# Kernel tuning notes

Measured on AMD Instinct MI355X. Metric: run time of the kernel, lower is better.

## Reference

```python
import jax, jax.numpy as jnp
import numpy as np

N, R, C_IN, C_OUT, MODES = 8, 256, 64, 64, 16


def setup_inputs() -> dict:
    key = jax.random.key(0)
    k1, k2, k3, k4, k5 = jax.random.split(key, 5)
    # xavier-like scale used in the torch init: gain/(in*out)*sqrt(in+out) folded into std
    std = (1.0 / (C_IN * C_OUT)) * np.sqrt(2.0)  # small, keeps spectra sane
    return {
        "X": jax.random.normal(k1, (N, R, R, C_IN), dtype=jnp.float32),
        "W_res": jax.random.normal(k2, (C_IN, C_OUT), dtype=jnp.float32) / np.sqrt(C_IN),
        "b_res": jax.random.normal(k3, (C_OUT,), dtype=jnp.float32) * 0.01,
        "fw0": jax.random.normal(k4, (C_IN, C_OUT, MODES, MODES, 2), dtype=jnp.float32) * std,
        "fw1": jax.random.normal(k5, (C_IN, C_OUT, MODES, MODES, 2), dtype=jnp.float32) * std,
    }


def reference(X, W_res, b_res, fw0, fw1):
    # X: [N, r, r, in_dim]
    n, r, _, _ = X.shape
    modes = fw0.shape[2]
    out_dim = fw0.shape[1]

    res = X @ W_res + b_res  # [N, r, r, out_dim]  (dropout p=0.0 -> identity)

    Xc = jnp.transpose(X, (0, 3, 1, 2))  # [N, in, r, r]
    X_ft = jnp.fft.rfft2(Xc, s=(r, r), norm="ortho")  # [N, in, r, r//2+1] complex

    w0 = fw0[..., 0] + 1j * fw0[..., 1]  # [in, out, m, m] complex
    w1 = fw1[..., 0] + 1j * fw1[..., 1]

    top = jnp.einsum("bixy,ioxy->boxy", X_ft[:, :, :modes, :modes], w0)
    bot = jnp.einsum("bixy,ioxy->boxy", X_ft[:, :, r - modes :, :modes], w1)

    out_ft = jnp.zeros((n, out_dim, r, r // 2 + 1), dtype=X_ft.dtype)
    out_ft = out_ft.at[:, :, :modes, :modes].set(top)
    out_ft = out_ft.at[:, :, r - modes :, :modes].set(bot)

    Xo = jnp.fft.irfft2(out_ft, s=(r, r), norm="ortho")  # [N, out, r, r] real
    Xo = jnp.transpose(Xo, (0, 2, 3, 1))  # [N, r, r, out]
    return jax.nn.silu(Xo + res)
```

## Files before the change

kernel.cpp:

```cpp
#include <hip/hip_runtime.h>
#include <math.h>

#define RDIM 256
#define CIN 64
#define COUT 64
#define MODES 16
#define NB 8

typedef short short8 __attribute__((ext_vector_type(8)));
typedef float f32x4 __attribute__((ext_vector_type(4)));

__device__ __forceinline__ unsigned short f2b(float f) {
    unsigned u = __builtin_bit_cast(unsigned, f);
    unsigned r = (u + 0x7FFFu + ((u >> 16) & 1u)) >> 16;
    return (unsigned short)r;
}

__global__ __launch_bounds__(256) void k_tf(unsigned short* __restrict__ Tf2,
                                            unsigned short* __restrict__ T2) {
    int e = blockIdx.x * 256 + (int)threadIdx.x;
    if (e < 8192) {
        int kyc = e >> 8, k = e & 255;
        int S = k >> 3, j = k & 7;
        int w = S >> 3, h = (S >> 2) & 1, q = S & 3;
        int y = w * 64 + q + 4 * (h * 8 + j);
        int ky = kyc >> 1;
        int p = (ky * y) & 255;
        float ang = (float)p * (float)(2.0 * M_PI / 256.0);
        float sz, cz;
        sincosf(ang, &sz, &cz);
        Tf2[e] = f2b((kyc & 1) ? -sz : cz);
    } else {
        int f = e - 8192;
        int r = f >> 9, k = f & 511;
        int S = k >> 3, j = k & 7;
        int w = S >> 4, bp = (S >> 3) & 1, a = S & 7;
        int d = j >> 1, c = j & 1;
        int x = w * 64 + bp + 8 * a + 2 * d;
        int m = r >> 1, cc = r & 1;
        int kx = (m < 16) ? m : (m + 224);
        int p = (kx * x) & 255;
        float ang = (float)p * (float)(2.0 * M_PI / 256.0);
        float sz, cz;
        sincosf(ang, &sz, &cz);
        float val = (cc == 0) ? (c ? sz : cz) : (c ? cz : -sz);
        T2[f] = f2b(val * (1.0f / 256.0f));
    }
}

__global__ __launch_bounds__(256) void k_wt(const float* __restrict__ fw0,
                                            const float* __restrict__ fw1,
                                            float2* __restrict__ WT) {
    __shared__ float2 Ls[16][257];
    int blk = blockIdx.x;
    int arr = blk >> 8;
    int tile = blk & 255;
    const float2* s2 = (const float2*)(arr ? fw1 : fw0);
    int t = (int)threadIdx.x;
    for (int e = t; e < 4096; e += 256) {
        int oo = e >> 8;
        int q = e & 255;
        Ls[oo][q] = s2[(size_t)(tile * 16 + oo) * 256 + q];
    }
    __syncthreads();
    int i = (tile * 16) >> 6;
    int o0 = (tile * 16) & 63;
    for (int e = t; e < 4096; e += 256) {
        int oo = e & 15;
        int q = e >> 4;
        int mx = q >> 4, ky = q & 15;
        int m = arr * 16 + mx;
        WT[((size_t)(m * 16 + ky) * 64 + i) * 64 + o0 + oo] = Ls[oo][q];
    }
}

__global__ __launch_bounds__(256) void k_prep(const float* __restrict__ Wres,
                                              unsigned short* __restrict__ WbT,
                                              unsigned short* __restrict__ Tg,
                                              unsigned short* __restrict__ A2) {
    int e = blockIdx.x * 256 + (int)threadIdx.x;
    if (e < 4096) {
        int o = e >> 6, k = e & 63;
        WbT[o * 64 + k] = f2b(Wres[k * 64 + o]);
    } else if (e < 12288) {
        int f = e - 4096;
        int y = f >> 5, kk = f & 31, ky = kk >> 1;
        int p = (ky * y) & 255;
        float ang = (float)p * (float)(2.0 * M_PI / 256.0);
        float sz, cz;
        sincosf(ang, &sz, &cz);
        Tg[f] = f2b((kk & 1) ? -sz : cz);
    } else {
        int f = e - 12288;
        int comp = f >> 14, g = f & 16383;
        int x = g >> 6, k = g & 63;
        int m = k >> 1, c = k & 1;
        int kx = (m < 16) ? m : (m + 224);
        int p = (kx * x) & 255;
        float ang = (float)p * (float)(2.0 * M_PI / 256.0);
        float sz, cz;
        sincosf(ang, &sz, &cz);
        float val = (comp == 0) ? (c ? -sz : cz) : (c ? cz : sz);
        A2[f] = f2b(val);
    }
}

__global__ __launch_bounds__(256) void k_fwd_y(const float* __restrict__ X,
                                               const unsigned short* __restrict__ Tf,
                                               float2* __restrict__ A) {
    __shared__ short8 Xb[64 * 32];
    int b = blockIdx.x >> 8;
    int x = blockIdx.x & 255;
    int t = (int)threadIdx.x;
    int w = t >> 6;
    int l = t & 63;
    int q = l >> 4;
    int f4 = l & 15;
    int i0 = f4 * 4;

    const float4* X4 = (const float4*)(X + ((size_t)(b * 256 + x)) * 256 * 64);
#pragma unroll
    for (int h = 0; h < 2; h++) {
        float4 v[8];
#pragma unroll
        for (int n = 0; n < 8; n++) {
            int y = w * 64 + q + 4 * (h * 8 + n);
            v[n] = X4[y * 16 + f4];
        }
        const float* vf = (const float*)v;
        int s = w * 8 + h * 4 + q;
#pragma unroll
        for (int di = 0; di < 4; di++) {
            int i = i0 + di;
            short8 hb;
#pragma unroll
            for (int j = 0; j < 8; j++) hb[j] = (short)f2b(vf[j * 4 + di]);
            Xb[i * 32 + (s ^ (i & 7))] = hb;
        }
    }
    __syncthreads();

    int m16 = l & 15;
    int quad = l >> 4;
    int iRow = w * 16 + m16;
    int isw = iRow & 7;

    f32x4 acc0 = (f32x4){0.f, 0.f, 0.f, 0.f};
    f32x4 acc1 = (f32x4){0.f, 0.f, 0.f, 0.f};
    const unsigned short* T0 = Tf + (size_t)m16 * 256 + quad * 8;
#pragma unroll
    for (int ks = 0; ks < 8; ks++) {
        short8 a0 = *(const short8*)(T0 + ks * 32);
        short8 a1 = *(const short8*)(T0 + 4096 + ks * 32);
        short8 bfrag = Xb[iRow * 32 + ((ks * 4 + quad) ^ isw)];
        acc0 = __builtin_amdgcn_mfma_f32_16x16x32_bf16(a0, bfrag, acc0, 0, 0, 0);
        acc1 = __builtin_amdgcn_mfma_f32_16x16x32_bf16(a1, bfrag, acc1, 0, 0, 0);
    }

    float2* Ab = A + ((size_t)(b * 16) * 256 + x) * 64;
    int ky0 = quad * 2;
    Ab[(size_t)(ky0)     * 16384 + iRow] = make_float2(acc0[0], acc0[1]);
    Ab[(size_t)(ky0 + 1) * 16384 + iRow] = make_float2(acc0[2], acc0[3]);
    Ab[(size_t)(ky0 + 8) * 16384 + iRow] = make_float2(acc1[0], acc1[1]);
    Ab[(size_t)(ky0 + 9) * 16384 + iRow] = make_float2(acc1[2], acc1[3]);
}

__global__ __launch_bounds__(256) void k_fwd_x(const float2* __restrict__ A,
                                               const unsigned short* __restrict__ T2,
                                               float2* __restrict__ C) {
    __shared__ short8 Bs[64 * 64];
    int bi = blockIdx.x;
    int b = bi >> 4;
    int ky = bi & 15;
    int t = (int)threadIdx.x;
    int w = t >> 6, l = t & 63;
    int i2 = (l & 31) * 2;
    int bp = l >> 5;
    const float4* A4 = (const float4*)(A + ((size_t)(b * 16 + ky)) * 256 * 64);
#pragma unroll
    for (int a = 0; a < 8; a++) {
        float4 v[4];
#pragma unroll
        for (int d4 = 0; d4 < 4; d4++) {
            int xx = w * 64 + bp + 8 * a + 2 * d4;
            v[d4] = A4[xx * 32 + (l & 31)];
        }
        int S = w * 16 + bp * 8 + a;
        short8 h0, h1;
        h0[0] = (short)f2b(v[0].x); h0[1] = (short)f2b(v[0].y);
        h0[2] = (short)f2b(v[1].x); h0[3] = (short)f2b(v[1].y);
        h0[4] = (short)f2b(v[2].x); h0[5] = (short)f2b(v[2].y);
        h0[6] = (short)f2b(v[3].x); h0[7] = (short)f2b(v[3].y);
        h1[0] = (short)f2b(v[0].z); h1[1] = (short)f2b(v[0].w);
        h1[2] = (short)f2b(v[1].z); h1[3] = (short)f2b(v[1].w);
        h1[4] = (short)f2b(v[2].z); h1[5] = (short)f2b(v[2].w);
        h1[6] = (short)f2b(v[3].z); h1[7] = (short)f2b(v[3].w);
        Bs[i2 * 64 + (S ^ (i2 & 7))] = h0;
        Bs[(i2 + 1) * 64 + (S ^ ((i2 + 1) & 7))] = h1;
    }
    __syncthreads();

    int m16 = l & 15, quad = l >> 4;
    int iRow = w * 16 + m16;
    int isw = iRow & 7;
    f32x4 acc[4];
#pragma unroll
    for (int mt = 0; mt < 4; mt++) acc[mt] = (f32x4){0.f, 0.f, 0.f, 0.f};
    const unsigned short* Tp = T2 + (size_t)m16 * 512 + quad * 8;
#pragma unroll
    for (int ks = 0; ks < 16; ks++) {
        short8 bfrag = Bs[iRow * 64 + ((ks * 4 + quad) ^ isw)];
#pragma unroll
        for (int mt = 0; mt < 4; mt++) {
            short8 af = *(const short8*)(Tp + mt * 8192 + ks * 32);
            acc[mt] = __builtin_amdgcn_mfma_f32_16x16x32_bf16(af, bfrag, acc[mt], 0, 0, 0);
        }
    }

    float2* Cb = C + ((size_t)(b * 16 + ky)) * 32 * 64;
#pragma unroll
    for (int mt = 0; mt < 4; mt++) {
        int m0 = mt * 8 + quad * 2;
        Cb[(size_t)m0 * 64 + iRow]       = make_float2(acc[mt][0], acc[mt][1]);
        Cb[(size_t)(m0 + 1) * 64 + iRow] = make_float2(acc[mt][2], acc[mt][3]);
    }
}

__global__ __launch_bounds__(256) void k_mix(const float2* __restrict__ C,
                                             const float2* __restrict__ WT,
                                             float2* __restrict__ D) {
    __shared__ float2 Ws[64 * 64];
    __shared__ float2 Cs[8 * 64];
    __shared__ float2 red[4 * 8 * 64];
    int bi = blockIdx.x;
    int ky = bi >> 5;
    int m = bi & 31;
    int t = (int)threadIdx.x;
    const float4* Wsrc = (const float4*)(WT + ((size_t)(m * 16 + ky)) * 4096);
    float4* Wd = (float4*)Ws;
    for (int e = t; e < 2048; e += 256) Wd[e] = Wsrc[e];
    for (int e = t; e < 512; e += 256) {
        int b = e >> 6;
        int i = e & 63;
        Cs[e] = C[(((size_t)b * 16 + ky) * 32 + m) * 64 + i];
    }
    __syncthreads();
    int o = t & 63;
    int ig = t >> 6;
    float dr[8], di[8];
#pragma unroll
    for (int b = 0; b < 8; b++) { dr[b] = 0.f; di[b] = 0.f; }
    for (int i2 = ig * 16; i2 < ig * 16 + 16; i2++) {
        float2 w = Ws[i2 * 64 + o];
#pragma unroll
        for (int b = 0; b < 8; b++) {
            float2 c = Cs[b * 64 + i2];
            dr[b] += c.x * w.x - c.y * w.y;
            di[b] += c.x * w.y + c.y * w.x;
        }
    }
#pragma unroll
    for (int b = 0; b < 8; b++) red[(ig * 8 + b) * 64 + o] = make_float2(dr[b], di[b]);
    __syncthreads();
    for (int e = t; e < 512; e += 256) {
        int b = e >> 6;
        int oo = e & 63;
        float2 s = red[b * 64 + oo];
        float2 s1 = red[(8 + b) * 64 + oo];
        float2 s2 = red[(16 + b) * 64 + oo];
        float2 s3 = red[(24 + b) * 64 + oo];
        D[(((size_t)b * 16 + ky) * 32 + m) * 64 + oo] =
            make_float2((s.x + s1.x) + (s2.x + s3.x), (s.y + s1.y) + (s2.y + s3.y));
    }
}

__global__ __launch_bounds__(256) void k_inv_x(const float2* __restrict__ D,
                                               const unsigned short* __restrict__ A2,
                                               float2* __restrict__ G) {
    __shared__ short8 Bd[64 * 8];
    int bi = blockIdx.x;
    int b = bi >> 5;
    int ky = (bi >> 1) & 15;
    int xh = bi & 1;
    int t = (int)threadIdx.x;
    int w = t >> 6, l = t & 63;
    const float2* Dp = D + ((size_t)(b * 16 + ky)) * 32 * 64;
    float2 dv[8];
#pragma unroll
    for (int s = 0; s < 8; s++) dv[s] = Dp[(size_t)(w * 8 + s) * 64 + l];
    short8 h0, h1;
    h0[0] = (short)f2b(dv[0].x); h0[1] = (short)f2b(dv[0].y);
    h0[2] = (short)f2b(dv[1].x); h0[3] = (short)f2b(dv[1].y);
    h0[4] = (short)f2b(dv[2].x); h0[5] = (short)f2b(dv[2].y);
    h0[6] = (short)f2b(dv[3].x); h0[7] = (short)f2b(dv[3].y);
    h1[0] = (short)f2b(dv[4].x); h1[1] = (short)f2b(dv[4].y);
    h1[2] = (short)f2b(dv[5].x); h1[3] = (short)f2b(dv[5].y);
    h1[4] = (short)f2b(dv[6].x); h1[5] = (short)f2b(dv[6].y);
    h1[6] = (short)f2b(dv[7].x); h1[7] = (short)f2b(dv[7].y);
    int sl = l & 7;
    Bd[l * 8 + ((2 * w) ^ sl)]     = h0;
    Bd[l * 8 + ((2 * w + 1) ^ sl)] = h1;
    __syncthreads();

    int m16 = l & 15, quad = l >> 4;
    int x0 = xh * 128 + w * 32;
    f32x4 acc[2][4][2];
#pragma unroll
    for (int mt = 0; mt < 2; mt++)
#pragma unroll
        for (int nt = 0; nt < 4; nt++)
#pragma unroll
            for (int c = 0; c < 2; c++) acc[mt][nt][c] = (f32x4){0.f, 0.f, 0.f, 0.f};

#pragma unroll
    for (int ks = 0; ks < 2; ks++) {
        short8 ar[2], ai[2];
#pragma unroll
        for (int mt = 0; mt < 2; mt++) {
            int xr = x0 + mt * 16 + m16;
            ar[mt] = *(const short8*)(A2 + (size_t)xr * 64 + ks * 32 + quad * 8);
            ai[mt] = *(const short8*)(A2 + 16384 + (size_t)xr * 64 + ks * 32 + quad * 8);
        }
#pragma unroll
        for (int nt = 0; nt < 4; nt++) {
            int o = nt * 16 + m16;
            short8 bf = Bd[o * 8 + ((ks * 4 + quad) ^ (o & 7))];
#pragma unroll
            for (int mt = 0; mt < 2; mt++) {
                acc[mt][nt][0] = __builtin_amdgcn_mfma_f32_16x16x32_bf16(ar[mt], bf, acc[mt][nt][0], 0, 0, 0);
                acc[mt][nt][1] = __builtin_amdgcn_mfma_f32_16x16x32_bf16(ai[mt], bf, acc[mt][nt][1], 0, 0, 0);
            }
        }
    }

#pragma unroll
    for (int mt = 0; mt < 2; mt++)
#pragma unroll
        for (int nt = 0; nt < 4; nt++) {
            int o = nt * 16 + m16;
#pragma unroll
            for (int r = 0; r < 4; r++) {
                int x = x0 + mt * 16 + quad * 4 + r;
                G[((size_t)(b * 256 + x) * 16 + ky) * 64 + o] =
                    make_float2(acc[mt][nt][0][r], acc[mt][nt][1][r]);
            }
        }
}

__global__ __launch_bounds__(256) void k_out(const float* __restrict__ X,
                                             const float2* __restrict__ G,
                                             const unsigned short* __restrict__ WbT,
                                             const unsigned short* __restrict__ Tg,
                                             const float* __restrict__ bres,
                                             float* __restrict__ out) {
    __shared__ unsigned short Bsp[64 * 32];
    int b = blockIdx.x >> 8;
    int x = blockIdx.x & 255;
    int t = (int)threadIdx.x;

    const float2* Gp = G + ((size_t)(b * 256 + x)) * 16 * 64;
    for (int e = t; e < 1024; e += 256) {
        int ky = e >> 6, o = e & 63;
        float2 g = Gp[e];
        float sc = (ky == 0) ? (1.0f / 256.0f) : (2.0f / 256.0f);
        Bsp[o * 32 + 2 * ky]     = f2b(g.x * sc);
        Bsp[o * 32 + 2 * ky + 1] = f2b(g.y * sc);
    }
    __syncthreads();

    int w = t >> 6;
    int l = t & 63;
    int m16 = l & 15;
    int quad = l >> 4;

    short8 bw0[4], bw1[4], bs[4];
    float br[4];
#pragma unroll
    for (int nt = 0; nt < 4; nt++) {
        int o = nt * 16 + m16;
        bw0[nt] = *(const short8*)(WbT + o * 64 + quad * 8);
        bw1[nt] = *(const short8*)(WbT + o * 64 + 32 + quad * 8);
        bs[nt]  = *(const short8*)(Bsp + o * 32 + quad * 8);
        br[nt]  = bres[o];
    }

    const float* Xrow = X + ((size_t)(b * 256 + x)) * 256 * 64;
    float* orow = out + ((size_t)(b * 256 + x)) * 256 * 64;

    f32x4 acc[4][4];
#pragma unroll
    for (int mt = 0; mt < 4; mt++)
#pragma unroll
        for (int nt = 0; nt < 4; nt++) acc[mt][nt] = (f32x4){0.f, 0.f, 0.f, 0.f};

#pragma unroll
    for (int mt = 0; mt < 4; mt++) {
        int y = w * 64 + mt * 16 + m16;
        const float4* xp = (const float4*)(Xrow + (size_t)y * 64 + quad * 8);
        float4 v0 = xp[0], v1 = xp[1];
        const float4* xq = (const float4*)(Xrow + (size_t)y * 64 + 32 + quad * 8);
        float4 v2 = xq[0], v3 = xq[1];
        short8 a0, a1;
        a0[0] = (short)f2b(v0.x); a0[1] = (short)f2b(v0.y);
        a0[2] = (short)f2b(v0.z); a0[3] = (short)f2b(v0.w);
        a0[4] = (short)f2b(v1.x); a0[5] = (short)f2b(v1.y);
        a0[6] = (short)f2b(v1.z); a0[7] = (short)f2b(v1.w);
        a1[0] = (short)f2b(v2.x); a1[1] = (short)f2b(v2.y);
        a1[2] = (short)f2b(v2.z); a1[3] = (short)f2b(v2.w);
        a1[4] = (short)f2b(v3.x); a1[5] = (short)f2b(v3.y);
        a1[6] = (short)f2b(v3.z); a1[7] = (short)f2b(v3.w);
        short8 aT = *(const short8*)(Tg + (size_t)y * 32 + quad * 8);
#pragma unroll
        for (int nt = 0; nt < 4; nt++) {
            acc[mt][nt] = __builtin_amdgcn_mfma_f32_16x16x32_bf16(a0, bw0[nt], acc[mt][nt], 0, 0, 0);
            acc[mt][nt] = __builtin_amdgcn_mfma_f32_16x16x32_bf16(a1, bw1[nt], acc[mt][nt], 0, 0, 0);
            acc[mt][nt] = __builtin_amdgcn_mfma_f32_16x16x32_bf16(aT, bs[nt],  acc[mt][nt], 0, 0, 0);
        }
    }

#pragma unroll
    for (int mt = 0; mt < 4; mt++) {
#pragma unroll
        for (int nt = 0; nt < 4; nt++) {
            int o = nt * 16 + m16;
#pragma unroll
            for (int r = 0; r < 4; r++) {
                int y = w * 64 + mt * 16 + quad * 4 + r;
                float v = acc[mt][nt][r] + br[nt];
                float sg = __builtin_amdgcn_rcpf(1.0f + __expf(-v));
                orow[(size_t)y * 64 + o] = v * sg;
            }
        }
    }
}

extern "C" void kernel_launch(void* const* d_in, const int* in_sizes, int n_in,
                              void* d_out, int out_size, void* d_ws, size_t ws_size,
                              hipStream_t stream) {
    const float* X    = (const float*)d_in[0];
    const float* Wres = (const float*)d_in[1];
    const float* bres = (const float*)d_in[2];
    const float* fw0  = (const float*)d_in[3];
    const float* fw1  = (const float*)d_in[4];
    float* out = (float*)d_out;

    float2* A  = (float2*)d_ws;
    float2* C  = A + 2097152;
    float2* D  = C + 262144;
    float2* WT = D + 262144;
    float2* G  = A;
    unsigned short* Tf2 = (unsigned short*)D;
    unsigned short* T2  = Tf2 + 8192;
    unsigned short* WbT = (unsigned short*)C;
    unsigned short* Tg  = WbT + 4096;
    unsigned short* A2  = Tg + 8192;

    k_wt<<<512, 256, 0, stream>>>(fw0, fw1, WT);
    k_tf<<<160, 256, 0, stream>>>(Tf2, T2);
    k_fwd_y<<<NB * 256, 256, 0, stream>>>(X, Tf2, A);
    k_fwd_x<<<128, 256, 0, stream>>>(A, T2, C);
    k_mix<<<16 * 32, 256, 0, stream>>>(C, WT, D);
    k_prep<<<176, 256, 0, stream>>>(Wres, WbT, Tg, A2);
    k_inv_x<<<256, 256, 0, stream>>>(D, A2, G);
    k_out<<<NB * 256, 256, 0, stream>>>(X, G, WbT, Tg, bres, out);
}
```

Measured before the change: 324.6 us.

## Merge table kernels, cache bf16 X, MFMA spectral mix, split fwd_x blocks

Merges the twiddle-table and residual-weight prep kernels into one launch. Spectral weights are pre-converted to bf16 in a real-block layout so the mode mixing runs on MFMA instead of scalar complex FMAs. The forward y-pass writes a bf16 copy of X for the output kernel to read, which halves its input traffic but adds a 32 MB write. k_fwd_x now splits channels across twice as many blocks to raise parallelism. The bf16 spectral mix may lose some accuracy.

```diff
diff --git a/kernel.cpp b/kernel.cpp
--- a/kernel.cpp
+++ b/kernel.cpp
@@ -16,8 +16,12 @@
     return (unsigned short)r;
 }
 
-__global__ __launch_bounds__(256) void k_tf(unsigned short* __restrict__ Tf2,
-                                            unsigned short* __restrict__ T2) {
+__global__ __launch_bounds__(256) void k_tab(const float* __restrict__ Wres,
+                                             unsigned short* __restrict__ Tf2,
+                                             unsigned short* __restrict__ T2,
+                                             unsigned short* __restrict__ WbT,
+                                             unsigned short* __restrict__ Tg,
+                                             unsigned short* __restrict__ A2) {
     int e = blockIdx.x * 256 + (int)threadIdx.x;
     if (e < 8192) {
         int kyc = e >> 8, k = e & 255;
@@ -30,7 +34,7 @@
         float sz, cz;
         sincosf(ang, &sz, &cz);
         Tf2[e] = f2b((kyc & 1) ? -sz : cz);
-    } else {
+    } else if (e < 40960) {
         int f = e - 8192;
         int r = f >> 9, k = f & 511;
         int S = k >> 3, j = k & 7;
@@ -45,45 +49,12 @@
         sincosf(ang, &sz, &cz);
         float val = (cc == 0) ? (c ? sz : cz) : (c ? cz : -sz);
         T2[f] = f2b(val * (1.0f / 256.0f));
-    }
-}
-
-__global__ __launch_bounds__(256) void k_wt(const float* __restrict__ fw0,
-                                            const float* __restrict__ fw1,
-                                            float2* __restrict__ WT) {
-    __shared__ float2 Ls[16][257];
-    int blk = blockIdx.x;
-    int arr = blk >> 8;
-    int tile = blk & 255;
-    const float2* s2 = (const float2*)(arr ? fw1 : fw0);
-    int t = (int)threadIdx.x;
-    for (int e = t; e < 4096; e += 256) {
-        int oo = e >> 8;
-        int q = e & 255;
-        Ls[oo][q] = s2[(size_t)(tile * 16 + oo) * 256 + q];
-    }
-    __syncthreads();
-    int i = (tile * 16) >> 6;
-    int o0 = (tile * 16) & 63;
-    for (int e = t; e < 4096; e += 256) {
-        int oo = e & 15;
-        int q = e >> 4;
-        int mx = q >> 4, ky = q & 15;
-        int m = arr * 16 + mx;
-        WT[((size_t)(m * 16 + ky) * 64 + i) * 64 + o0 + oo] = Ls[oo][q];
-    }
-}
-
-__global__ __launch_bounds__(256) void k_prep(const float* __restrict__ Wres,
-                                              unsigned short* __restrict__ WbT,
-                                              unsigned short* __restrict__ Tg,
-                                              unsigned short* __restrict__ A2) {
-    int e = blockIdx.x * 256 + (int)threadIdx.x;
-    if (e < 4096) {
-        int o = e >> 6, k = e & 63;
+    } else if (e < 45056) {
+        int f = e - 40960;
+        int o = f >> 6, k = f & 63;
         WbT[o * 64 + k] = f2b(Wres[k * 64 + o]);
-    } else if (e < 12288) {
-        int f = e - 4096;
+    } else if (e < 53248) {
+        int f = e - 45056;
         int y = f >> 5, kk = f & 31, ky = kk >> 1;
         int p = (ky * y) & 255;
         float ang = (float)p * (float)(2.0 * M_PI / 256.0);
@@ -91,7 +62,7 @@
         sincosf(ang, &sz, &cz);
         Tg[f] = f2b((kk & 1) ? -sz : cz);
     } else {
-        int f = e - 12288;
+        int f = e - 53248;
         int comp = f >> 14, g = f & 16383;
         int x = g >> 6, k = g & 63;
         int m = k >> 1, c = k & 1;
@@ -105,9 +76,50 @@
     }
 }
 
+__global__ __launch_bounds__(256) void k_wt(const float* __restrict__ fw0,
+                                            const float* __restrict__ fw1,
+                                            unsigned short* __restrict__ WTb) {
+    __shared__ float2 Ls[64 * 134];
+    int bi = blockIdx.x;
+    int arr = bi >> 7;
+    int iq = (bi >> 3) & 15;
+    int oq = (bi >> 1) & 3;
+    int h = bi & 1;
+    int i0 = iq * 4, o0 = oq * 16;
+    const float4* fw4 = (const float4*)(arr ? fw1 : fw0);
+    int t = (int)threadIdx.x;
+#pragma unroll
+    for (int n = 0; n < 16; n++) {
+        int idx = n * 256 + t;
+        int io = idx >> 6, fi = idx & 63;
+        int i_loc = io >> 4, o_loc = io & 15;
+        float4 v = fw4[(size_t)((i0 + i_loc) * 64 + o0 + o_loc) * 128 + h * 64 + fi];
+        ((float4*)Ls)[io * 67 + fi] = v;
+    }
+    __syncthreads();
+#pragma unroll
+    for (int n = 0; n < 16; n++) {
+        int u = n * 256 + t;
+        int o_loc = u & 15, ky = (u >> 4) & 15, mm = (u >> 8) & 7, var = u >> 11;
+        int qL = mm * 16 + ky;
+        short8 hh;
+#pragma unroll
+        for (int j = 0; j < 8; j++) {
+            int i_loc = j >> 1, c = j & 1;
+            float2 wv = Ls[(i_loc * 16 + o_loc) * 134 + qL];
+            float val = var ? (c ? wv.x : wv.y) : (c ? -wv.y : wv.x);
+            hh[j] = (short)f2b(val);
+        }
+        int m = arr * 16 + h * 8 + mm;
+        int o = o0 + o_loc;
+        *(short8*)(WTb + (size_t)(m * 16 + ky) * 16384 + var * 8192 + iq * 512 + o * 8) = hh;
+    }
+}
+
 __global__ __launch_bounds__(256) void k_fwd_y(const float* __restrict__ X,
                                                const unsigned short* __restrict__ Tf,
-                                               float2* __restrict__ A) {
+                                               float2* __restrict__ A,
+                                               unsigned short* __restrict__ Xbf) {
     __shared__ short8 Xb[64 * 32];
     int b = blockIdx.x >> 8;
     int x = blockIdx.x & 255;
@@ -119,6 +131,7 @@
     int i0 = f4 * 4;
 
     const float4* X4 = (const float4*)(X + ((size_t)(b * 256 + x)) * 256 * 64);
+    unsigned short* Xrow = Xbf + ((size_t)(b * 256 + x)) * 16384;
 #pragma unroll
     for (int h = 0; h < 2; h++) {
         float4 v[8];
@@ -126,6 +139,12 @@
         for (int n = 0; n < 8; n++) {
             int y = w * 64 + q + 4 * (h * 8 + n);
             v[n] = X4[y * 16 + f4];
+        }
+#pragma unroll
+        for (int n = 0; n < 8; n++) {
+            int y = w * 64 + q + 4 * (h * 8 + n);
+            *(ushort4*)(Xrow + (size_t)y * 64 + i0) =
+                make_ushort4(f2b(v[n].x), f2b(v[n].y), f2b(v[n].z), f2b(v[n].w));
         }
         const float* vf = (const float*)v;
         int s = w * 8 + h * 4 + q;
@@ -168,22 +187,25 @@
 __global__ __launch_bounds__(256) void k_fwd_x(const float2* __restrict__ A,
                                                const unsigned short* __restrict__ T2,
                                                float2* __restrict__ C) {
-    __shared__ short8 Bs[64 * 64];
+    __shared__ short8 Bs[32 * 64];
     int bi = blockIdx.x;
-    int b = bi >> 4;
-    int ky = bi & 15;
+    int b = bi >> 5;
+    int ky = (bi >> 1) & 15;
+    int ih = bi & 1;
     int t = (int)threadIdx.x;
     int w = t >> 6, l = t & 63;
-    int i2 = (l & 31) * 2;
-    int bp = l >> 5;
-    const float4* A4 = (const float4*)(A + ((size_t)(b * 16 + ky)) * 256 * 64);
-#pragma unroll
-    for (int a = 0; a < 8; a++) {
+    int ip = l & 15;
+    int bp = (l >> 4) & 1;
+    int ab = l >> 5;
+    const float4* A4 = (const float4*)(A + ((size_t)(b * 16 + ky)) * 16384);
+#pragma unroll
+    for (int aa = 0; aa < 4; aa++) {
+        int a = ab * 4 + aa;
         float4 v[4];
 #pragma unroll
         for (int d4 = 0; d4 < 4; d4++) {
             int xx = w * 64 + bp + 8 * a + 2 * d4;
-            v[d4] = A4[xx * 32 + (l & 31)];
+            v[d4] = A4[xx * 32 + ih * 16 + ip];
         }
         int S = w * 16 + bp * 8 + a;
         short8 h0, h1;
@@ -195,82 +217,85 @@
         h1[2] = (short)f2b(v[1].z); h1[3] = (short)f2b(v[1].w);
         h1[4] = (short)f2b(v[2].z); h1[5] = (short)f2b(v[2].w);
         h1[6] = (short)f2b(v[3].z); h1[7] = (short)f2b(v[3].w);
-        Bs[i2 * 64 + (S ^ (i2 & 7))] = h0;
-        Bs[(i2 + 1) * 64 + (S ^ ((i2 + 1) & 7))] = h1;
+        int iL0 = ip * 2, iL1 = iL0 + 1;
+        Bs[iL0 * 64 + (S ^ (iL0 & 7))] = h0;
+        Bs[iL1 * 64 + (S ^ (iL1 & 7))] = h1;
     }
     __syncthreads();
 
     int m16 = l & 15, quad = l >> 4;
-    int iRow = w * 16 + m16;
-    int isw = iRow & 7;
-    f32x4 acc[4];
-#pragma unroll
-    for (int mt = 0; mt < 4; mt++) acc[mt] = (f32x4){0.f, 0.f, 0.f, 0.f};
-    const unsigned short* Tp = T2 + (size_t)m16 * 512 + quad * 8;
+    f32x4 acc[2];
+    acc[0] = (f32x4){0.f, 0.f, 0.f, 0.f};
+    acc[1] = (f32x4){0.f, 0.f, 0.f, 0.f};
+    const unsigned short* Tp = T2 + (size_t)(w * 16 + m16) * 512 + quad * 8;
 #pragma unroll
     for (int ks = 0; ks < 16; ks++) {
-        short8 bfrag = Bs[iRow * 64 + ((ks * 4 + quad) ^ isw)];
-#pragma unroll
-        for (int mt = 0; mt < 4; mt++) {
-            short8 af = *(const short8*)(Tp + mt * 8192 + ks * 32);
-            acc[mt] = __builtin_amdgcn_mfma_f32_16x16x32_bf16(af, bfrag, acc[mt], 0, 0, 0);
-        }
-    }
-
-    float2* Cb = C + ((size_t)(b * 16 + ky)) * 32 * 64;
-#pragma unroll
-    for (int mt = 0; mt < 4; mt++) {
-        int m0 = mt * 8 + quad * 2;
-        Cb[(size_t)m0 * 64 + iRow]       = make_float2(acc[mt][0], acc[mt][1]);
-        Cb[(size_t)(m0 + 1) * 64 + iRow] = make_float2(acc[mt][2], acc[mt][3]);
+        short8 af = *(const short8*)(Tp + ks * 32);
+#pragma unroll
+        for (int nt = 0; nt < 2; nt++) {
+            int iL = nt * 16 + m16;
+            short8 bfr = Bs[iL * 64 + ((ks * 4 + quad) ^ (iL & 7))];
+            acc[nt] = __builtin_amdgcn_mfma_f32_16x16x32_bf16(af, bfr, acc[nt], 0, 0, 0);
+        }
+    }
+
+    float2* Cb = C + ((size_t)(b * 16 + ky)) * 2048;
+    int m0 = w * 8 + quad * 2;
+#pragma unroll
+    for (int nt = 0; nt < 2; nt++) {
+        int ig = ih * 32 + nt * 16 + m16;
+        Cb[(size_t)m0 * 64 + ig]       = make_float2(acc[nt][0], acc[nt][1]);
+        Cb[(size_t)(m0 + 1) * 64 + ig] = make_float2(acc[nt][2], acc[nt][3]);
     }
 }
 
 __global__ __launch_bounds__(256) void k_mix(const float2* __restrict__ C,
-                                             const float2* __restrict__ WT,
+                                             const unsigned short* __restrict__ WTb,
                                              float2* __restrict__ D) {
-    __shared__ float2 Ws[64 * 64];
-    __shared__ float2 Cs[8 * 64];
-    __shared__ float2 red[4 * 8 * 64];
+    __shared__ float Csf[8 * 132];
     int bi = blockIdx.x;
-    int ky = bi >> 5;
-    int m = bi & 31;
-    int t = (int)threadIdx.x;
-    const float4* Wsrc = (const float4*)(WT + ((size_t)(m * 16 + ky)) * 4096);
-    float4* Wd = (float4*)Ws;
-    for (int e = t; e < 2048; e += 256) Wd[e] = Wsrc[e];
-    for (int e = t; e < 512; e += 256) {
-        int b = e >> 6;
-        int i = e & 63;
-        Cs[e] = C[(((size_t)b * 16 + ky) * 32 + m) * 64 + i];
-    }
-    __syncthreads();
-    int o = t & 63;
-    int ig = t >> 6;
-    float dr[8], di[8];
-#pragma unroll
-    for (int b = 0; b < 8; b++) { dr[b] = 0.f; di[b] = 0.f; }
-    for (int i2 = ig * 16; i2 < ig * 16 + 16; i2++) {
-        float2 w = Ws[i2 * 64 + o];
-#pragma unroll
-        for (int b = 0; b < 8; b++) {
-            float2 c = Cs[b * 64 + i2];
-            dr[b] += c.x * w.x - c.y * w.y;
-            di[b] += c.x * w.y + c.y * w.x;
-        }
-    }
-#pragma unroll
-    for (int b = 0; b < 8; b++) red[(ig * 8 + b) * 64 + o] = make_float2(dr[b], di[b]);
-    __syncthreads();
-    for (int e = t; e < 512; e += 256) {
-        int b = e >> 6;
-        int oo = e & 63;
-        float2 s = red[b * 64 + oo];
-        float2 s1 = red[(8 + b) * 64 + oo];
-        float2 s2 = red[(16 + b) * 64 + oo];
-        float2 s3 = red[(24 + b) * 64 + oo];
-        D[(((size_t)b * 16 + ky) * 32 + m) * 64 + oo] =
-            make_float2((s.x + s1.x) + (s2.x + s3.x), (s.y + s1.y) + (s2.y + s3.y));
+    int ky = bi >> 5, m = bi & 31;
+    int t = (int)threadIdx.x;
+    {
+        int bq = t >> 5;
+        int e = t & 31;
+        const float4* src = (const float4*)(C + (((size_t)bq * 16 + ky) * 32 + m) * 64);
+        ((float4*)Csf)[bq * 33 + e] = src[e];
+    }
+    __syncthreads();
+    int w = t >> 6, l = t & 63;
+    int var = w >> 1, ntb = (w & 1) * 2;
+    int m16 = l & 15, quad = l >> 4;
+    const unsigned short* Wp = WTb + (size_t)(m * 16 + ky) * 16384 + var * 8192;
+    const float* cp0 = Csf + (m16 & 7) * 132 + quad * 8;
+    f32x4 acc[2];
+    acc[0] = (f32x4){0.f, 0.f, 0.f, 0.f};
+    acc[1] = (f32x4){0.f, 0.f, 0.f, 0.f};
+#pragma unroll
+    for (int ks = 0; ks < 4; ks++) {
+        const float* cp = cp0 + ks * 32;
+        short8 af;
+#pragma unroll
+        for (int j = 0; j < 8; j++) af[j] = (short)f2b(cp[j]);
+        int oct = ks * 4 + quad;
+#pragma unroll
+        for (int n2 = 0; n2 < 2; n2++) {
+            int o = (ntb + n2) * 16 + m16;
+            short8 bfr = *(const short8*)(Wp + oct * 512 + o * 8);
+            acc[n2] = __builtin_amdgcn_mfma_f32_16x16x32_bf16(af, bfr, acc[n2], 0, 0, 0);
+        }
+    }
+    if (quad < 2) {
+#pragma unroll
+        for (int n2 = 0; n2 < 2; n2++) {
+            int o = (ntb + n2) * 16 + m16;
+#pragma unroll
+            for (int r = 0; r < 4; r++) {
+                int bb = quad * 4 + r;
+                float* dp = (float*)&D[(((size_t)bb * 16 + ky) * 32 + m) * 64 + o];
+                dp[var] = acc[n2][r];
+            }
+        }
     }
 }
 
@@ -284,7 +309,7 @@
     int xh = bi & 1;
     int t = (int)threadIdx.x;
     int w = t >> 6, l = t & 63;
-    const float2* Dp = D + ((size_t)(b * 16 + ky)) * 32 * 64;
+    const float2* Dp = D + ((size_t)(b * 16 + ky)) * 2048;
     float2 dv[8];
 #pragma unroll
     for (int s = 0; s < 8; s++) dv[s] = Dp[(size_t)(w * 8 + s) * 64 + l];
@@ -347,7 +372,7 @@
         }
 }
 
-__global__ __launch_bounds__(256) void k_out(const float* __restrict__ X,
+__global__ __launch_bounds__(256) void k_out(const unsigned short* __restrict__ Xbf,
                                              const float2* __restrict__ G,
                                              const unsigned short* __restrict__ WbT,
                                              const unsigned short* __restrict__ Tg,
@@ -384,7 +409,7 @@
         br[nt]  = bres[o];
     }
 
-    const float* Xrow = X + ((size_t)(b * 256 + x)) * 256 * 64;
+    const unsigned short* Xrow = Xbf + ((size_t)(b * 256 + x)) * 16384;
     float* orow = out + ((size_t)(b * 256 + x)) * 256 * 64;
 
     f32x4 acc[4][4];
@@ -396,19 +421,8 @@
 #pragma unroll
     for (int mt = 0; mt < 4; mt++) {
         int y = w * 64 + mt * 16 + m16;
-        const float4* xp = (const float4*)(Xrow + (size_t)y * 64 + quad * 8);
-        float4 v0 = xp[0], v1 = xp[1];
-        const float4* xq = (const float4*)(Xrow + (size_t)y * 64 + 32 + quad * 8);
-        float4 v2 = xq[0], v3 = xq[1];
-        short8 a0, a1;
-        a0[0] = (short)f2b(v0.x); a0[1] = (short)f2b(v0.y);
-        a0[2] = (short)f2b(v0.z); a0[3] = (short)f2b(v0.w);
-        a0[4] = (short)f2b(v1.x); a0[5] = (short)f2b(v1.y);
-        a0[6] = (short)f2b(v1.z); a0[7] = (short)f2b(v1.w);
-        a1[0] = (short)f2b(v2.x); a1[1] = (short)f2b(v2.y);
-        a1[2] = (short)f2b(v2.z); a1[3] = (short)f2b(v2.w);
-        a1[4] = (short)f2b(v3.x); a1[5] = (short)f2b(v3.y);
-        a1[6] = (short)f2b(v3.z); a1[7] = (short)f2b(v3.w);
+        short8 a0 = *(const short8*)(Xrow + (size_t)y * 64 + quad * 8);
+        short8 a1 = *(const short8*)(Xrow + (size_t)y * 64 + 32 + quad * 8);
         short8 aT = *(const short8*)(Tg + (size_t)y * 32 + quad * 8);
 #pragma unroll
         for (int nt = 0; nt < 4; nt++) {
@@ -444,23 +458,23 @@
     const float* fw1  = (const float*)d_in[4];
     float* out = (float*)d_out;
 
-    float2* A  = (float2*)d_ws;
-    float2* C  = A + 2097152;
-    float2* D  = C + 262144;
-    float2* WT = D + 262144;
-    float2* G  = A;
-    unsigned short* Tf2 = (unsigned short*)D;
+    float2* A = (float2*)d_ws;
+    float2* C = A + 2097152;
+    float2* D = C + 262144;
+    unsigned short* WTb = (unsigned short*)(D + 262144);
+    unsigned short* Xbf = WTb + 8388608;
+    unsigned short* Tf2 = Xbf + 33554432;
     unsigned short* T2  = Tf2 + 8192;
-    unsigned short* WbT = (unsigned short*)C;
+    unsigned short* WbT = T2 + 32768;
     unsigned short* Tg  = WbT + 4096;
     unsigned short* A2  = Tg + 8192;
-
-    k_wt<<<512, 256, 0, stream>>>(fw0, fw1, WT);
-    k_tf<<<160, 256, 0, stream>>>(Tf2, T2);
-    k_fwd_y<<<NB * 256, 256, 0, stream>>>(X, Tf2, A);
-    k_fwd_x<<<128, 256, 0, stream>>>(A, T2, C);
-    k_mix<<<16 * 32, 256, 0, stream>>>(C, WT, D);
-    k_prep<<<176, 256, 0, stream>>>(Wres, WbT, Tg, A2);
+    float2* G = A;
+
+    k_tab<<<336, 256, 0, stream>>>(Wres, Tf2, T2, WbT, Tg, A2);
+    k_wt<<<256, 256, 0, stream>>>(fw0, fw1, WTb);
+    k_fwd_y<<<NB * 256, 256, 0, stream>>>(X, Tf2, A, Xbf);
+    k_fwd_x<<<256, 256, 0, stream>>>(A, T2, C);
+    k_mix<<<512, 256, 0, stream>>>(C, WTb, D);
     k_inv_x<<<256, 256, 0, stream>>>(D, A2, G);
-    k_out<<<NB * 256, 256, 0, stream>>>(X, G, WbT, Tg, bres, out);
-}
+    k_out<<<NB * 256, 256, 0, stream>>>(Xbf, G, WbT, Tg, bres, out);
+}
```

After: 310.8 us. 1.04x faster.
